# Performance work log

Hardware: AMD Instinct MI355X
Metric: run time of the kernel (lower is better)

The kernel has to match this reference:

```python
import jax, jax.numpy as jnp
import numpy as np

EPS = 1e-6  # flax LayerNorm default
ROPE_BASE = 10000.0

def _ln(x, scale, bias):
    m = jnp.mean(x, axis=-1, keepdims=True)
    v = jnp.mean(jnp.square(x - m), axis=-1, keepdims=True)
    return (x - m) * jax.lax.rsqrt(v + EPS) * scale + bias

def _rope_cache(u, v, head_dim):
    # P = head_dim//2//2 pairs per axis
    P = head_dim // 4
    freqs = jnp.arange(P, dtype=jnp.float32) / (P - 1 + 1e-9)
    inv = 1.0 / ROPE_BASE ** freqs
    ang_x = jnp.einsum('nl,f->nlf', u, inv)
    ang_y = jnp.einsum('nl,f->nlf', v, inv)
    return jnp.cos(ang_x), jnp.sin(ang_x), jnp.cos(ang_y), jnp.sin(ang_y)

def _rope_apply(q, cos_x, sin_x, cos_y, sin_y):
    n, L, H, D = q.shape
    q = q.reshape(n, L, H, D // 2, 2)
    P = D // 4
    qx, qy = q[..., :P, :], q[..., P:, :]
    def rot(qp, c, s):
        c = c[:, :, None, :]
        s = s[:, :, None, :]
        x, y = qp[..., 0], qp[..., 1]
        return jnp.stack([x * c - y * s, x * s + y * c], axis=-1)
    return jnp.concatenate([rot(qx, cos_x, sin_x), rot(qy, cos_y, sin_y)], axis=-2).reshape(n, L, H, D)

def setup_inputs():
    key = jax.random.key(0)
    ks = jax.random.split(key, 12)
    N, HW, CIN = 8, 384, 3
    P, W, DPT, H, HD, MLP = 16, 768, 4, 12, 64, 3072
    s = 0.02
    return {
        'image': jax.random.normal(ks[0], (N, HW, HW, CIN), jnp.float32),
        'conv_kernel': jax.random.normal(ks[1], (P, P, CIN, W), jnp.float32) * s,
        'conv_bias': jnp.zeros((W,), jnp.float32),
        'ln1_scale': jnp.ones((DPT, W), jnp.float32),
        'ln1_bias': jnp.zeros((DPT, W), jnp.float32),
        'wq': jax.random.normal(ks[2], (DPT, W, H, HD), jnp.float32) * s,
        'bq': jnp.zeros((DPT, H, HD), jnp.float32),
        'wk': jax.random.normal(ks[3], (DPT, W, H, HD), jnp.float32) * s,
        'bk': jnp.zeros((DPT, H, HD), jnp.float32),
        'wv': jax.random.normal(ks[4], (DPT, W, H, HD), jnp.float32) * s,
        'bv': jnp.zeros((DPT, H, HD), jnp.float32),
        'wo': jax.random.normal(ks[5], (DPT, H, HD, W), jnp.float32) * s,
        'bo': jnp.zeros((DPT, W), jnp.float32),
        'ln2_scale': jnp.ones((DPT, W), jnp.float32),
        'ln2_bias': jnp.zeros((DPT, W), jnp.float32),
        'w1': jax.random.normal(ks[6], (DPT, W, MLP), jnp.float32) * s,
        'b1': jnp.zeros((DPT, MLP), jnp.float32),
        'w2': jax.random.normal(ks[7], (DPT, MLP, W), jnp.float32) * s,
        'b2': jnp.zeros((DPT, W), jnp.float32),
        'lnf_scale': jnp.ones((W,), jnp.float32),
        'lnf_bias': jnp.zeros((W,), jnp.float32),
    }

def reference(image, conv_kernel, conv_bias, ln1_scale, ln1_bias,
              wq, bq, wk, bk, wv, bv, wo, bo,
              ln2_scale, ln2_bias, w1, b1, w2, b2, lnf_scale, lnf_bias):
    patch = conv_kernel.shape[0]
    # patch-embedding conv, stride=patch, VALID padding (NHWC/HWIO)
    x = jax.lax.conv_general_dilated(
        image, conv_kernel, window_strides=(patch, patch), padding='VALID',
        dimension_numbers=('NHWC', 'HWIO', 'NHWC')) + conv_bias
    n, h, w, c = x.shape
    L = h * w
    x = x.reshape(n, L, c)

    depth, _, H, HD = wq.shape
    # RoPE 2D coordinates for square grid (default path when rope_uv is None)
    ys, xs = jnp.mgrid[:h, :w]
    u = jnp.tile(((xs.reshape(-1) + 0.5) / w)[None, :], [n, 1])
    v = jnp.tile(((ys.reshape(-1) + 0.5) / h)[None, :], [n, 1])
    cos_x, sin_x, cos_y, sin_y = _rope_cache(u, v, HD)

    scale = 1.0 / jnp.sqrt(jnp.float32(HD))
    for l in range(depth):
        y = _ln(x, ln1_scale[l], ln1_bias[l])
        q = jnp.einsum('nld,dhk->nlhk', y, wq[l]) + bq[l]
        k = jnp.einsum('nld,dhk->nlhk', y, wk[l]) + bk[l]
        vv = jnp.einsum('nld,dhk->nlhk', y, wv[l]) + bv[l]
        q = _rope_apply(q, cos_x, sin_x, cos_y, sin_y)
        k = _rope_apply(k, cos_x, sin_x, cos_y, sin_y)
        logits = jnp.einsum('nqhd,nkhd->nhqk', q, k) * scale
        attn = jax.nn.softmax(logits, axis=-1)
        o = jnp.einsum('nhqk,nkhd->nqhd', attn, vv)
        y = jnp.einsum('nqhd,hdo->nqo', o, wo[l]) + bo[l]
        x = x + y
        y = _ln(x, ln2_scale[l], ln2_bias[l])
        y = jax.nn.gelu(jnp.einsum('nld,df->nlf', y, w1[l]) + b1[l])
        y = jnp.einsum('nlf,fd->nld', y, w2[l]) + b2[l]
        x = x + y

    x = _ln(x, lnf_scale, lnf_bias)  # encoder_norm
    return jnp.mean(x, axis=1)       # gap pooling -> [n, width]
```

## Files before the change

kernel.cpp:

```cpp
#include <hip/hip_runtime.h>
#include <hip/hip_bf16.h>

typedef __hip_bfloat16 bf16;
typedef __bf16 bf16x8 __attribute__((ext_vector_type(8)));
typedef float f32x4  __attribute__((ext_vector_type(4)));

#define NBATCH 8
#define LTOK   576
#define NT     4608
#define CW     768
#define NH     12
#define HDIM   64
#define DEPTH  4
#define MLPW   3072
#define GRIDP  24
#define IMGS   384
#define QKVW   2304

static __device__ __forceinline__ unsigned bfpair(float a, float b){
    bf16 x = __float2bfloat16(a), y = __float2bfloat16(b);
    return ((unsigned)*(unsigned short*)&y << 16) | *(unsigned short*)&x;
}
static __device__ __forceinline__ float b2f(bf16 v){ return __bfloat162float(v); }

static __device__ __forceinline__ int xcd_swizzle(int orig, int nwg){
    int q = nwg >> 3, r = nwg & 7;
    int xcd = orig & 7, j = orig >> 3;
    int base = (xcd < r) ? xcd*(q+1) : r*(q+1) + (xcd-r)*q;
    return base + j;
}

static __device__ __forceinline__ void gl_lds16(const bf16* g, bf16* l){
    __builtin_amdgcn_global_load_lds(
        (const __attribute__((address_space(1))) unsigned int*)(const void*)g,
        (__attribute__((address_space(3))) unsigned int*)(void*)l, 16, 0, 0);
}

__global__ void rope_cache_kernel(float* __restrict__ rc){
    int idx = blockIdx.x*256 + threadIdx.x;
    if (idx >= LTOK*16) return;
    int l = idx >> 4, f = idx & 15;
    int py = l / GRIDP, px = l % GRIDP;
    float u = (px + 0.5f) / (float)GRIDP;
    float v = (py + 0.5f) / (float)GRIDP;
    float fr = (float)f / (15.0f + 1e-9f);
    float inv = expf(-fr * 9.210340371976184f);
    float sx, cx, sy, cy;
    sincosf(u * inv, &sx, &cx);
    sincosf(v * inv, &sy, &cy);
    rc[idx]         = cx;
    rc[idx + 9216]  = sx;
    rc[idx + 18432] = cy;
    rc[idx + 27648] = sy;
}

__global__ void patch_gather(const float* __restrict__ img, bf16* __restrict__ p){
    int idx = blockIdx.x*256 + threadIdx.x;
    int t = idx / CW, kk = idx % CW;
    int n = t / LTOK, l = t % LTOK;
    int py = l / GRIDP, px = l % GRIDP;
    int i = kk / 48, r = kk % 48, j = r / 3, c = r % 3;
    p[idx] = __float2bfloat16(img[((size_t)(n*IMGS + py*16 + i)*IMGS + px*16 + j)*3 + c]);
}

__global__ __launch_bounds__(256) void wtrans_b(const float* __restrict__ in, bf16* __restrict__ out,
                                                int K, int N, size_t inStride, size_t outStride){
    in  += blockIdx.z * inStride;
    out += blockIdx.z * outStride;
    __shared__ float t[32][33];
    const int n0 = blockIdx.x*32, k0 = blockIdx.y*32;
    const int tx = threadIdx.x & 31, ty = threadIdx.x >> 5;
    #pragma unroll
    for (int r = 0; r < 4; ++r)
        t[ty + 8*r][tx] = in[(size_t)(k0 + ty + 8*r)*N + n0 + tx];
    __syncthreads();
    #pragma unroll
    for (int r = 0; r < 4; ++r)
        out[(size_t)(n0 + ty + 8*r)*K + k0 + tx] = __float2bfloat16(t[tx][ty + 8*r]);
}

__global__ void bias_pack(const float* __restrict__ bq, const float* __restrict__ bk,
                          const float* __restrict__ bv, float* __restrict__ o){
    int idx = blockIdx.x*256 + threadIdx.x;
    int l = idx / QKVW, r = idx % QKVW;
    const float* src = (r < 768) ? (bq + l*768 + r) :
                       (r < 1536) ? (bk + l*768 + r - 768) : (bv + l*768 + r - 1536);
    o[idx] = *src;
}

static __device__ __forceinline__ float gelu_tanh(float x){
    float x3 = x*x*x;
    return 0.5f*x*(1.0f + tanhf(0.7978845608028654f*(x + 0.044715f*x3)));
}

template<int EPI, typename TC>
__global__ __launch_bounds__(256) void gemm_a(const bf16* __restrict__ A, int lda,
                                              const bf16* __restrict__ B, int ldb,
                                              const float* __restrict__ bias,
                                              TC* __restrict__ C, int ldc, int K){
    __shared__ bf16 As[128*64];
    __shared__ bf16 Bs[64*64];
    const int tid = threadIdx.x;
    const int w = tid >> 6, l = tid & 63;
    const int quad = l >> 4, lr = l & 15;
    const int wm = w & 1, wn = w >> 1;

    const int nwg = gridDim.x * gridDim.y;
    const int swz = xcd_swizzle(blockIdx.y * gridDim.x + blockIdx.x, nwg);
    const int rowT = (swz / gridDim.x) * 128;
    const int colT = (swz % gridDim.x) * 64;

    const int srow = l >> 3;
    const int schk = (l & 7) ^ (srow & 7);
    f32x4 acc[4][2];
    #pragma unroll
    for (int i = 0; i < 4; ++i)
        #pragma unroll
        for (int j = 0; j < 2; ++j) acc[i][j] = (f32x4){0.f,0.f,0.f,0.f};

    for (int k0 = 0; k0 < K; k0 += 64){
        const bf16* Ab = A + (size_t)rowT*lda + k0;
        const bf16* Bb = B + (size_t)colT*ldb + k0;
        #pragma unroll
        for (int t = 0; t < 4; ++t){
            int s = w*4 + t;
            gl_lds16(Ab + (size_t)(s*8 + srow)*lda + schk*8, As + s*512);
        }
        #pragma unroll
        for (int t = 0; t < 2; ++t){
            int s = w*2 + t;
            gl_lds16(Bb + (size_t)(s*8 + srow)*ldb + schk*8, Bs + s*512);
        }
        __syncthreads();
        #pragma unroll
        for (int kh = 0; kh < 2; ++kh){
            bf16x8 af[4], bfr[2];
            #pragma unroll
            for (int i = 0; i < 4; ++i){
                int r = wm*64 + i*16 + lr;
                af[i] = *(const bf16x8*)(As + r*64 + (((kh*4 + quad) ^ (r & 7))*8));
            }
            #pragma unroll
            for (int j = 0; j < 2; ++j){
                int r = wn*32 + j*16 + lr;
                bfr[j] = *(const bf16x8*)(Bs + r*64 + (((kh*4 + quad) ^ (r & 7))*8));
            }
            #pragma unroll
            for (int i = 0; i < 4; ++i)
                #pragma unroll
                for (int j = 0; j < 2; ++j)
                    acc[i][j] = __builtin_amdgcn_mfma_f32_16x16x32_bf16(af[i], bfr[j], acc[i][j], 0, 0, 0);
        }
        __syncthreads();
    }

    #pragma unroll
    for (int i = 0; i < 4; ++i){
        #pragma unroll
        for (int j = 0; j < 2; ++j){
            const int row = rowT + wm*64 + i*16 + quad*4;
            const int col = colT + wn*32 + j*16 + lr;
            const float bb = bias ? bias[col] : 0.f;
            #pragma unroll
            for (int r = 0; r < 4; ++r){
                float val = acc[i][j][r] + bb;
                TC* cp = C + (size_t)(row + r)*ldc + col;
                if (EPI == 2) val = gelu_tanh(val);
                if (EPI == 1) val += *(float*)cp;
                if (EPI == 0 || EPI == 2) *(bf16*)cp = __float2bfloat16(val);
                else                      *(float*)cp = val;
            }
        }
    }
}

__global__ __launch_bounds__(256) void ln_wave(const float* __restrict__ x,
                                               const float* __restrict__ sc,
                                               const float* __restrict__ bs,
                                               bf16* __restrict__ y){
    const int tid = threadIdx.x, w = tid >> 6, l = tid & 63;
    const int t = blockIdx.x*4 + w;
    const float4* xr = (const float4*)(x + (size_t)t*CW);
    float4 a[3];
    #pragma unroll
    for (int i = 0; i < 3; ++i) a[i] = xr[l + 64*i];
    float s = 0.f;
    #pragma unroll
    for (int i = 0; i < 3; ++i) s += a[i].x + a[i].y + a[i].z + a[i].w;
    #pragma unroll
    for (int off = 1; off < 64; off <<= 1) s += __shfl_xor(s, off);
    const float m = s * (1.0f/768.0f);
    float vs = 0.f;
    #pragma unroll
    for (int i = 0; i < 3; ++i){
        float dx = a[i].x-m, dy = a[i].y-m, dz = a[i].z-m, dw = a[i].w-m;
        vs += dx*dx + dy*dy + dz*dz + dw*dw;
    }
    #pragma unroll
    for (int off = 1; off < 64; off <<= 1) vs += __shfl_xor(vs, off);
    const float rs = rsqrtf(vs*(1.0f/768.0f) + 1e-6f);
    const float4* scp = (const float4*)sc;
    const float4* bsp = (const float4*)bs;
    uint2* yr = (uint2*)(y + (size_t)t*CW);
    #pragma unroll
    for (int i = 0; i < 3; ++i){
        float4 sv = scp[l + 64*i], bv = bsp[l + 64*i];
        float r0 = (a[i].x-m)*rs*sv.x + bv.x;
        float r1 = (a[i].y-m)*rs*sv.y + bv.y;
        float r2 = (a[i].z-m)*rs*sv.z + bv.z;
        float r3 = (a[i].w-m)*rs*sv.w + bv.w;
        yr[l + 64*i] = make_uint2(bfpair(r0,r1), bfpair(r2,r3));
    }
}

__global__ void rope_qk(bf16* __restrict__ qkv, const float* __restrict__ rc){
    int idx = blockIdx.x*256 + threadIdx.x;
    int tok = idx / 768;
    int r = idx % 768;
    int rr, base;
    if (r < 384){ base = 0; rr = r; } else { base = 768; rr = r - 384; }
    int hh = rr >> 5, p = rr & 31;
    int l = tok % LTOK;
    float c, s;
    if (p < 16){ c = rc[l*16 + p];            s = rc[9216 + l*16 + p]; }
    else       { c = rc[18432 + l*16 + p-16]; s = rc[27648 + l*16 + p-16]; }
    bf16* pp = qkv + (size_t)tok*QKVW + base + hh*64 + 2*p;
    unsigned u = *(unsigned*)pp;
    bf16 lo = *(bf16*)&u; unsigned short hi16 = u >> 16; bf16 hi = *(bf16*)&hi16;
    float x = b2f(lo), y = b2f(hi);
    *(unsigned*)pp = bfpair(x*c - y*s, x*s + y*c);
}

__global__ __launch_bounds__(256) void vtrans(const bf16* __restrict__ qkv, bf16* __restrict__ vT){
    __shared__ bf16 tile[64][72];
    const int t0 = blockIdx.x*64, hI = blockIdx.y, nI = blockIdx.z;
    const size_t base = ((size_t)nI*LTOK + t0)*QKVW + 1536 + hI*64;
    const int tid = threadIdx.x;
    #pragma unroll
    for (int i = 0; i < 2; ++i){
        int g = i*256 + tid, r = g >> 3, c = g & 7;
        *(uint4*)&tile[r][c*8] = *(const uint4*)(qkv + base + (size_t)r*QKVW + c*8);
    }
    __syncthreads();
    const size_t obase = ((size_t)(nI*NH + hI)*64)*576 + t0;
    #pragma unroll
    for (int i = 0; i < 2; ++i){
        int g = i*256 + tid, d = g >> 3, c = g & 7;
        bf16 tmp[8];
        #pragma unroll
        for (int j = 0; j < 8; ++j) tmp[j] = tile[c*8 + j][d];
        *(uint4*)(vT + obase + (size_t)d*576 + c*8) = *(uint4*)tmp;
    }
}

__global__ __launch_bounds__(256) void attn_flash(const bf16* __restrict__ qkv,
                                                  const bf16* __restrict__ vT,
                                                  bf16* __restrict__ o){
    __shared__ bf16 Ks[64*72];
    __shared__ bf16 Vs[64*72];
    __shared__ bf16 Ps[64*72];
    __shared__ float alph[64];
    __shared__ float lsum[64];
    const int tid = threadIdx.x;
    const int w = tid >> 6, l = tid & 63;
    const int quad = l >> 4, lr = l & 15;

    const int nwg = gridDim.x * gridDim.y * gridDim.z;
    const int orig = (blockIdx.z * gridDim.y + blockIdx.y) * gridDim.x + blockIdx.x;
    const int swz = xcd_swizzle(orig, nwg);
    const int q0 = (swz % gridDim.x) * 64;
    const int t2 = swz / gridDim.x;
    const int hI = t2 % gridDim.y;
    const int nI = t2 / gridDim.y;

    const size_t tokBase = (size_t)nI * LTOK;
    const int off = hI * 64;
    const size_t vbase = ((size_t)(nI*NH + hI)*64)*576;

    bf16x8 qf[2];
    #pragma unroll
    for (int kh = 0; kh < 2; ++kh)
        qf[kh] = *(const bf16x8*)(qkv + (tokBase + q0 + w*16 + lr)*QKVW + off + kh*32 + quad*8);

    f32x4 oacc[4];
    #pragma unroll
    for (int j = 0; j < 4; ++j) oacc[j] = (f32x4){0.f,0.f,0.f,0.f};
    float m_run = -3.0e38f, l_run = 0.f;

    for (int ch = 0; ch < 9; ++ch){
        __syncthreads();
        #pragma unroll
        for (int i = 0; i < 2; ++i){
            int g = i*256 + tid, r = g >> 3, c = g & 7;
            *(uint4*)(Ks + r*72 + c*8) =
                *(const uint4*)(qkv + (tokBase + ch*64 + r)*QKVW + 768 + off + c*8);
        }
        #pragma unroll
        for (int i = 0; i < 2; ++i){
            int g = i*256 + tid, d = g >> 3, c = g & 7;
            *(uint4*)(Vs + d*72 + c*8) = *(const uint4*)(vT + vbase + (size_t)d*576 + ch*64 + c*8);
        }
        __syncthreads();

        f32x4 st[4];
        #pragma unroll
        for (int t = 0; t < 4; ++t){
            st[t] = (f32x4){0.f,0.f,0.f,0.f};
            #pragma unroll
            for (int kh = 0; kh < 2; ++kh){
                bf16x8 kf = *(const bf16x8*)(Ks + (t*16 + lr)*72 + kh*32 + quad*8);
                st[t] = __builtin_amdgcn_mfma_f32_16x16x32_bf16(kf, qf[kh], st[t], 0, 0, 0);
            }
        }
        float lm = -3.0e38f;
        #pragma unroll
        for (int t = 0; t < 4; ++t)
            #pragma unroll
            for (int r = 0; r < 4; ++r){
                st[t][r] *= 0.125f;
                lm = fmaxf(lm, st[t][r]);
            }
        lm = fmaxf(lm, __shfl_xor(lm, 16));
        lm = fmaxf(lm, __shfl_xor(lm, 32));
        float mn = fmaxf(m_run, lm);
        float alpha = __expf(m_run - mn);
        m_run = mn;
        float ls = 0.f;
        #pragma unroll
        for (int t = 0; t < 4; ++t)
            #pragma unroll
            for (int r = 0; r < 4; ++r){
                float p = __expf(st[t][r] - mn);
                st[t][r] = p; ls += p;
            }
        ls += __shfl_xor(ls, 16);
        ls += __shfl_xor(ls, 32);
        l_run = l_run*alpha + ls;
        if ((tid & 48) == 0) alph[w*16 + lr] = alpha;
        #pragma unroll
        for (int t = 0; t < 4; ++t)
            #pragma unroll
            for (int r = 0; r < 4; ++r)
                Ps[(w*16 + lr)*72 + t*16 + quad*4 + r] = __float2bfloat16(st[t][r]);
        float af[4];
        #pragma unroll
        for (int r = 0; r < 4; ++r) af[r] = alph[w*16 + quad*4 + r];
        #pragma unroll
        for (int j = 0; j < 4; ++j)
            #pragma unroll
            for (int r = 0; r < 4; ++r) oacc[j][r] *= af[r];
        #pragma unroll
        for (int kh = 0; kh < 2; ++kh){
            bf16x8 pf = *(const bf16x8*)(Ps + (w*16 + lr)*72 + kh*32 + quad*8);
            #pragma unroll
            for (int j = 0; j < 4; ++j){
                bf16x8 vf = *(const bf16x8*)(Vs + (j*16 + lr)*72 + kh*32 + quad*8);
                oacc[j] = __builtin_amdgcn_mfma_f32_16x16x32_bf16(pf, vf, oacc[j], 0, 0, 0);
            }
        }
    }

    if ((tid & 48) == 0) lsum[w*16 + lr] = l_run;
    float linv[4];
    #pragma unroll
    for (int r = 0; r < 4; ++r) linv[r] = 1.0f / lsum[w*16 + quad*4 + r];
    #pragma unroll
    for (int j = 0; j < 4; ++j)
        #pragma unroll
        for (int r = 0; r < 4; ++r)
            o[(tokBase + q0 + w*16 + quad*4 + r)*CW + off + j*16 + lr] =
                __float2bfloat16(oacc[j][r] * linv[r]);
}

__global__ void mean_kernel(const bf16* __restrict__ y, float* __restrict__ out){
    int c = blockIdx.x*256 + threadIdx.x;
    int n = blockIdx.y;
    float s = 0.f;
    for (int l = 0; l < LTOK; ++l) s += b2f(y[((size_t)n*LTOK + l)*CW + c]);
    out[n*CW + c] = s * (1.0f/576.0f);
}

extern "C" void kernel_launch(void* const* d_in, const int* in_sizes, int n_in,
                              void* d_out, int out_size, void* d_ws, size_t ws_size,
                              hipStream_t stream){
    const float* image = (const float*)d_in[0];
    const float* convk = (const float*)d_in[1];
    const float* convb = (const float*)d_in[2];
    const float* ln1s  = (const float*)d_in[3];
    const float* ln1b  = (const float*)d_in[4];
    const float* wq    = (const float*)d_in[5];
    const float* bq    = (const float*)d_in[6];
    const float* wk    = (const float*)d_in[7];
    const float* bk    = (const float*)d_in[8];
    const float* wv    = (const float*)d_in[9];
    const float* bv    = (const float*)d_in[10];
    const float* wo    = (const float*)d_in[11];
    const float* bo    = (const float*)d_in[12];
    const float* ln2s  = (const float*)d_in[13];
    const float* ln2b  = (const float*)d_in[14];
    const float* w1    = (const float*)d_in[15];
    const float* b1    = (const float*)d_in[16];
    const float* w2    = (const float*)d_in[17];
    const float* b2    = (const float*)d_in[18];
    const float* lnfs  = (const float*)d_in[19];
    const float* lnfb  = (const float*)d_in[20];
    float* out = (float*)d_out;

    const size_t u = (size_t)NT*CW;
    float* ws    = (float*)d_ws;
    float* ropeC = ws;
    float* bqkvA = ws + 36864;
    float* x     = bqkvA + 4*QKVW;
    bf16*  y     = (bf16*)(x + u);
    bf16*  qkv   = y + u;
    bf16*  o     = qkv + (size_t)NT*QKVW;
    bf16*  h     = o + u;
    bf16*  vT    = h + (size_t)NT*MLPW;
    bf16*  convT = vT + u;
    bf16*  wqkvT = convT + 589824;
    bf16*  woT   = wqkvT + (size_t)4*QKVW*CW;
    bf16*  w1T   = woT + (size_t)4*CW*CW;
    bf16*  w2T   = w1T + (size_t)4*CW*MLPW;

    rope_cache_kernel<<<36, 256, 0, stream>>>(ropeC);
    patch_gather<<<(NT*CW)/256, 256, 0, stream>>>(image, y);
    bias_pack<<<36, 256, 0, stream>>>(bq, bk, bv, bqkvA);
    wtrans_b<<<dim3(24,24,1), 256, 0, stream>>>(convk, convT, CW, CW, 0, 0);
    wtrans_b<<<dim3(24,24,4), 256, 0, stream>>>(wq, wqkvT,           CW, CW, (size_t)CW*CW, (size_t)QKVW*CW);
    wtrans_b<<<dim3(24,24,4), 256, 0, stream>>>(wk, wqkvT + 589824,  CW, CW, (size_t)CW*CW, (size_t)QKVW*CW);
    wtrans_b<<<dim3(24,24,4), 256, 0, stream>>>(wv, wqkvT + 1179648, CW, CW, (size_t)CW*CW, (size_t)QKVW*CW);
    wtrans_b<<<dim3(24,24,4), 256, 0, stream>>>(wo, woT,             CW, CW, (size_t)CW*CW, (size_t)CW*CW);
    wtrans_b<<<dim3(96,24,4), 256, 0, stream>>>(w1, w1T,  CW, MLPW, (size_t)CW*MLPW, (size_t)CW*MLPW);
    wtrans_b<<<dim3(24,96,4), 256, 0, stream>>>(w2, w2T, MLPW,  CW, (size_t)CW*MLPW, (size_t)CW*MLPW);

    gemm_a<3,float><<<dim3(12,36), 256, 0, stream>>>(y, CW, convT, CW, convb, x, CW, CW);

    for (int l = 0; l < DEPTH; ++l){
        ln_wave<<<NT/4, 256, 0, stream>>>(x, ln1s + l*CW, ln1b + l*CW, y);
        gemm_a<0,bf16><<<dim3(36,36), 256, 0, stream>>>(y, CW, wqkvT + (size_t)l*QKVW*CW, CW,
                                                        bqkvA + l*QKVW, qkv, QKVW, CW);
        rope_qk<<<(NT*768)/256, 256, 0, stream>>>(qkv, ropeC);
        vtrans<<<dim3(9, NH, NBATCH), 256, 0, stream>>>(qkv, vT);
        attn_flash<<<dim3(9, NH, NBATCH), 256, 0, stream>>>(qkv, vT, o);
        gemm_a<1,float><<<dim3(12,36), 256, 0, stream>>>(o, CW, woT + (size_t)l*CW*CW, CW,
                                                         bo + l*CW, x, CW, CW);
        ln_wave<<<NT/4, 256, 0, stream>>>(x, ln2s + l*CW, ln2b + l*CW, y);
        gemm_a<2,bf16><<<dim3(48,36), 256, 0, stream>>>(y, CW, w1T + (size_t)l*CW*MLPW, CW,
                                                        b1 + l*MLPW, h, MLPW, CW);
        gemm_a<1,float><<<dim3(12,36), 256, 0, stream>>>(h, MLPW, w2T + (size_t)l*CW*MLPW, MLPW,
                                                         b2 + l*CW, x, CW, MLPW);
    }
    ln_wave<<<NT/4, 256, 0, stream>>>(x, lnfs, lnfb, y);
    mean_kernel<<<dim3(3, NBATCH), 256, 0, stream>>>(y, out);
}
```

Baseline: 1.039 ms.

## Double-buffer LDS tiles in GEMM to overlap global loads with MFMA

The bf16 GEMM kernel now keeps two shared-memory buffers for the A and B tiles. It issues the global-to-LDS loads for the next K step before computing on the current one, and it precomputes the per-thread source pointers once outside the loop. The aim is to hide global load latency behind the MFMA work and to drop one barrier per K iteration. In exchange, shared memory per block doubles, which may reduce occupancy.

Result: slower. 1.071 ms (+3.1%).

```diff
diff --git a/kernel.cpp b/kernel.cpp
--- a/kernel.cpp
+++ b/kernel.cpp
@@ -98,8 +98,8 @@
                                               const bf16* __restrict__ B, int ldb,
                                               const float* __restrict__ bias,
                                               TC* __restrict__ C, int ldc, int K){
-    __shared__ bf16 As[128*64];
-    __shared__ bf16 Bs[64*64];
+    __shared__ bf16 As[2][128*64];
+    __shared__ bf16 Bs[2][64*64];
     const int tid = threadIdx.x;
     const int w = tid >> 6, l = tid & 63;
     const int quad = l >> 4, lr = l & 15;
@@ -112,38 +112,47 @@
 
     const int srow = l >> 3;
     const int schk = (l & 7) ^ (srow & 7);
+
+    const bf16* Ap[4];
+    const bf16* Bp[2];
+    #pragma unroll
+    for (int t = 0; t < 4; ++t)
+        Ap[t] = A + (size_t)(rowT + (w*4+t)*8 + srow)*lda + schk*8;
+    #pragma unroll
+    for (int t = 0; t < 2; ++t)
+        Bp[t] = B + (size_t)(colT + (w*2+t)*8 + srow)*ldb + schk*8;
+
+    auto STAGE = [&](int k0, int buf){
+        #pragma unroll
+        for (int t = 0; t < 4; ++t) gl_lds16(Ap[t] + k0, &As[buf][(w*4+t)*512]);
+        #pragma unroll
+        for (int t = 0; t < 2; ++t) gl_lds16(Bp[t] + k0, &Bs[buf][(w*2+t)*512]);
+    };
+
     f32x4 acc[4][2];
     #pragma unroll
     for (int i = 0; i < 4; ++i)
         #pragma unroll
         for (int j = 0; j < 2; ++j) acc[i][j] = (f32x4){0.f,0.f,0.f,0.f};
 
+    STAGE(0, 0);
+    __syncthreads();
+
+    int cur = 0;
     for (int k0 = 0; k0 < K; k0 += 64){
-        const bf16* Ab = A + (size_t)rowT*lda + k0;
-        const bf16* Bb = B + (size_t)colT*ldb + k0;
-        #pragma unroll
-        for (int t = 0; t < 4; ++t){
-            int s = w*4 + t;
-            gl_lds16(Ab + (size_t)(s*8 + srow)*lda + schk*8, As + s*512);
-        }
-        #pragma unroll
-        for (int t = 0; t < 2; ++t){
-            int s = w*2 + t;
-            gl_lds16(Bb + (size_t)(s*8 + srow)*ldb + schk*8, Bs + s*512);
-        }
-        __syncthreads();
+        if (k0 + 64 < K) STAGE(k0 + 64, cur ^ 1);
         #pragma unroll
         for (int kh = 0; kh < 2; ++kh){
             bf16x8 af[4], bfr[2];
             #pragma unroll
             for (int i = 0; i < 4; ++i){
                 int r = wm*64 + i*16 + lr;
-                af[i] = *(const bf16x8*)(As + r*64 + (((kh*4 + quad) ^ (r & 7))*8));
+                af[i] = *(const bf16x8*)(&As[cur][r*64 + (((kh*4 + quad) ^ (r & 7))*8)]);
             }
             #pragma unroll
             for (int j = 0; j < 2; ++j){
                 int r = wn*32 + j*16 + lr;
-                bfr[j] = *(const bf16x8*)(Bs + r*64 + (((kh*4 + quad) ^ (r & 7))*8));
+                bfr[j] = *(const bf16x8*)(&Bs[cur][r*64 + (((kh*4 + quad) ^ (r & 7))*8)]);
             }
             #pragma unroll
             for (int i = 0; i < 4; ++i)
@@ -152,6 +161,7 @@
                     acc[i][j] = __builtin_amdgcn_mfma_f32_16x16x32_bf16(af[i], bfr[j], acc[i][j], 0, 0, 0);
         }
         __syncthreads();
+        cur ^= 1;
     }
 
     #pragma unroll
```
